# Performance work log

Measured on AMD Instinct MI355X. Metric: run time of the kernel, lower is better.

Reference implementation:

```python
import jax, jax.numpy as jnp
import numpy as np

B, S, HMODEL = 2, 4096, 2048
NH, HD, K = 16, 128, 4
RMS_EPS = 1e-5
L2_EPS = 1e-6


def setup_inputs() -> dict:
    key = jax.random.key(0)
    ks = jax.random.split(key, 10)
    def p(k, shape, std=0.02):
        return jax.random.normal(k, shape, jnp.float32) * std
    return {
        "x": jax.random.normal(ks[0], (B, S, HMODEL), jnp.float32),
        "Wq": p(ks[1], (NH * HD, HMODEL)),
        "Wk": p(ks[2], (NH * HD, HMODEL)),
        "Wv": p(ks[3], (NH * HD, HMODEL)),
        "Wb": p(ks[4], (NH, HMODEL)),
        "Wo": p(ks[5], (HMODEL, NH * HD)),
        "conv_q": p(ks[6], (NH * HD, K), 0.3),
        "conv_k": p(ks[7], (NH * HD, K), 0.3),
        "conv_v": p(ks[8], (NH * HD, K), 0.3),
        "rms_w": jnp.ones((HD,), jnp.float32),
    }


def causal_conv_silu(x, w):
    # depthwise causal conv1d: x [B,S,C], w [C,K]; out[t] = sum_i w[:,i]*x[t-K+1+i]
    Kw = w.shape[1]
    xp = jnp.pad(x, ((0, 0), (Kw - 1, 0), (0, 0)))
    out = sum(w[:, i] * xp[:, i:i + x.shape[1], :] for i in range(Kw))
    return jax.nn.silu(out)


def l2norm(x):
    return x * jax.lax.rsqrt(jnp.sum(x * x, axis=-1, keepdims=True) + L2_EPS)


def reference(x, Wq, Wk, Wv, Wb, Wo, conv_q, conv_k, conv_v, rms_w):
    b, s, _ = x.shape
    nh = Wb.shape[0]
    hd = Wq.shape[0] // nh

    q = causal_conv_silu(x @ Wq.T, conv_q)
    k = causal_conv_silu(x @ Wk.T, conv_k)
    v = causal_conv_silu(x @ Wv.T, conv_v)

    q = q.reshape(b, s, nh, hd)
    k = k.reshape(b, s, nh, hd)
    v = v.reshape(b, s, nh, hd)
    beta = jax.nn.sigmoid(x @ Wb.T)  # [B,S,NH]

    # qk l2 norm in kernel + default scale d_k^-0.5 on q
    q = l2norm(q) * (hd ** -0.5)
    k = l2norm(k)

    # delta rule recurrence: state [B,NH,HD,HD] (d_k x d_v)
    qT = jnp.moveaxis(q, 1, 0)  # [S,B,NH,HD]
    kT = jnp.moveaxis(k, 1, 0)
    vT = jnp.moveaxis(v, 1, 0)
    bT = jnp.moveaxis(beta, 1, 0)  # [S,B,NH]

    def step(state, inp):
        qt, kt, vt, bt = inp
        pred = jnp.einsum('bhd,bhdv->bhv', kt, state)
        delta = bt[..., None] * (vt - pred)
        state = state + jnp.einsum('bhd,bhv->bhdv', kt, delta)
        ot = jnp.einsum('bhd,bhdv->bhv', qt, state)
        return state, ot

    s0 = jnp.zeros((b, nh, hd, hd), x.dtype)
    _, o = jax.lax.scan(step, s0, (qT, kT, vT, bT))
    o = jnp.moveaxis(o, 0, 1)  # [B,S,NH,HD]

    # RMSNorm over head_dim
    o = o * jax.lax.rsqrt(jnp.mean(o * o, axis=-1, keepdims=True) + RMS_EPS) * rms_w

    o = o.reshape(b, s, nh * hd) @ Wo.T
    return o
```

## Files before the change

kernel.cpp:

```cpp
#include <hip/hip_runtime.h>

#define DI __device__ __forceinline__

constexpr int Bb = 2, Ss = 4096, Hm = 2048, NHh = 16, HDd = 128;
constexpr int ROWS = Bb * Ss;
constexpr int QKVN = 3 * Hm;
constexpr int CC = 64;
constexpr int NC = Ss / CC;

typedef __bf16 bf16x8 __attribute__((ext_vector_type(8)));
typedef float f32x4 __attribute__((ext_vector_type(4)));

DI unsigned short f2bf(float f) {
  unsigned int u = __float_as_uint(f);
  u = u + 0x7FFFu + ((u >> 16) & 1u);
  return (unsigned short)(u >> 16);
}
DI float bf2f(unsigned int u) { return __uint_as_float(u << 16); }
DI void ld_bf8(const unsigned short* p, float* f) {
  uint4 u = *(const uint4*)p;
  f[0] = bf2f(u.x & 0xffffu); f[1] = bf2f(u.x >> 16);
  f[2] = bf2f(u.y & 0xffffu); f[3] = bf2f(u.y >> 16);
  f[4] = bf2f(u.z & 0xffffu); f[5] = bf2f(u.z >> 16);
  f[6] = bf2f(u.w & 0xffffu); f[7] = bf2f(u.w >> 16);
}

DI void gld16(const unsigned short* g, unsigned short* l) {
  __builtin_amdgcn_global_load_lds(
      (const __attribute__((address_space(1))) unsigned int*)g,
      (__attribute__((address_space(3))) unsigned int*)l, 16, 0, 0);
}

DI void bar_lds() {
  asm volatile("s_waitcnt lgkmcnt(0)" ::: "memory");
  __builtin_amdgcn_s_barrier();
}

__global__ void cast_x_k(const float* __restrict__ x, unsigned short* __restrict__ xb) {
  int i = blockIdx.x * 256 + threadIdx.x;
  float4 f = ((const float4*)x)[i];
  ushort4 u;
  u.x = f2bf(f.x); u.y = f2bf(f.y); u.z = f2bf(f.z); u.w = f2bf(f.w);
  ((ushort4*)xb)[i] = u;
}

__global__ void cast_w_k(const float* __restrict__ Wq, const float* __restrict__ Wk,
                         const float* __restrict__ Wv, const float* __restrict__ Wo,
                         unsigned short* __restrict__ wqkv, unsigned short* __restrict__ wo) {
  const int W1 = Hm * Hm;
  int idx = blockIdx.x * 256 + threadIdx.x;
  for (int r = 0; r < 4; r++) {
    int i = idx + r * W1;
    if (i < W1)            wqkv[i] = f2bf(Wq[i]);
    else if (i < 2 * W1)   wqkv[i] = f2bf(Wk[i - W1]);
    else if (i < 3 * W1)   wqkv[i] = f2bf(Wv[i - 2 * W1]);
    else                   wo[i - 3 * W1] = f2bf(Wo[i - 3 * W1]);
  }
}

template <bool BF16_OUT>
__global__ __launch_bounds__(256) void gemm_bt(const unsigned short* __restrict__ A,
                                               const unsigned short* __restrict__ Bm,
                                               void* __restrict__ Cout,
                                               int M, int N, int Kd) {
  __shared__ __align__(16) unsigned short As[128 * 32];
  __shared__ __align__(16) unsigned short Bs[128 * 32];
  int tid = threadIdx.x;
  int bm = blockIdx.y * 128, bn = blockIdx.x * 128;
  int wave = tid >> 6, lane = tid & 63;
  int wm = (wave >> 1) * 64, wn = (wave & 1) * 64;
  int lm = lane & 15, lq = lane >> 4;
  f32x4 acc[4][4] = {};
  int sr = lane >> 2;
  int sc = (lane & 3) * 8;

  for (int k0 = 0; k0 < Kd; k0 += 32) {
    __syncthreads();
#pragma unroll
    for (int i = 0; i < 2; i++) {
      int inst = (wave << 1) + i;
      int r = inst * 16 + sr;
      gld16(&A[(size_t)(bm + r) * Kd + k0 + sc], &As[inst * 512]);
      gld16(&Bm[(size_t)(bn + r) * Kd + k0 + sc], &Bs[inst * 512]);
    }
    __syncthreads();
    bf16x8 af[4], bfr[4];
#pragma unroll
    for (int i = 0; i < 4; i++) af[i]  = *(const bf16x8*)&As[(wm + i * 16 + lm) * 32 + lq * 8];
#pragma unroll
    for (int j = 0; j < 4; j++) bfr[j] = *(const bf16x8*)&Bs[(wn + j * 16 + lm) * 32 + lq * 8];
#pragma unroll
    for (int i = 0; i < 4; i++)
#pragma unroll
      for (int j = 0; j < 4; j++)
        acc[i][j] = __builtin_amdgcn_mfma_f32_16x16x32_bf16(af[i], bfr[j], acc[i][j], 0, 0, 0);
  }
#pragma unroll
  for (int i = 0; i < 4; i++)
#pragma unroll
    for (int j = 0; j < 4; j++) {
      int row = bm + wm + i * 16 + lq * 4;
      int col = bn + wn + j * 16 + lm;
#pragma unroll
      for (int r = 0; r < 4; r++) {
        if (BF16_OUT)
          ((unsigned short*)Cout)[(size_t)(row + r) * N + col] = f2bf(acc[i][j][r]);
        else
          ((float*)Cout)[(size_t)(row + r) * N + col] = acc[i][j][r];
      }
    }
}

__global__ __launch_bounds__(256) void conv_k(const unsigned short* __restrict__ qkvh,
                                              const float* __restrict__ cwq,
                                              const float* __restrict__ cwk,
                                              const float* __restrict__ cwv,
                                              unsigned short* __restrict__ qb,
                                              unsigned short* __restrict__ kb,
                                              unsigned short* __restrict__ vb) {
  __shared__ __align__(16) float sm[32 * 260];
  __shared__ float fac[64];
  int tid = threadIdx.x;
  int cblk = blockIdx.x * 256;
  int s0 = blockIdx.y * 32;
  int z = blockIdx.z;
  int sel = z >> 1, b = z & 1;
  const float* cw = sel == 0 ? cwq : (sel == 1 ? cwk : cwv);
  int c = cblk + tid;
  float4 w = ((const float4*)cw)[c];
  const unsigned short* in = qkvh + (size_t)b * Ss * QKVN + sel * Hm + c;
  float x0 = (s0 >= 3) ? bf2f(in[(size_t)(s0 - 3) * QKVN]) : 0.f;
  float x1 = (s0 >= 2) ? bf2f(in[(size_t)(s0 - 2) * QKVN]) : 0.f;
  float x2 = (s0 >= 1) ? bf2f(in[(size_t)(s0 - 1) * QKVN]) : 0.f;
  for (int si = 0; si < 32; si++) {
    float x3 = bf2f(in[(size_t)(s0 + si) * QKVN]);
    float a = w.x * x0 + w.y * x1 + w.z * x2 + w.w * x3;
    sm[si * 260 + tid] = a / (1.f + __expf(-a));
    x0 = x1; x1 = x2; x2 = x3;
  }
  __syncthreads();
  if (sel < 2) {
    int si = tid >> 3, p = tid & 7;
    const float* row = &sm[si * 260 + p * 32];
    float ss = 0.f;
#pragma unroll
    for (int j = 0; j < 32; j += 4) {
      float4 v4 = *(const float4*)(row + j);
      ss += v4.x * v4.x + v4.y * v4.y + v4.z * v4.z + v4.w * v4.w;
    }
    ss += __shfl_xor(ss, 1);
    ss += __shfl_xor(ss, 2);
    float f = rsqrtf(ss + 1e-6f);
    if (sel == 0) f *= 0.08838834764831845f;
    if ((p & 3) == 0) fac[si * 2 + (p >> 2)] = f;
  }
  __syncthreads();
  unsigned short* outp = sel == 0 ? qb : (sel == 1 ? kb : vb);
  int hl = tid >> 7;
  for (int si = 0; si < 32; si++) {
    float val = sm[si * 260 + tid];
    if (sel < 2) val *= fac[si * 2 + hl];
    outp[(size_t)(b * Ss + s0 + si) * Hm + cblk + tid] = f2bf(val);
  }
}

__global__ __launch_bounds__(256) void beta_k(const float* __restrict__ x,
                                              const float* __restrict__ Wbm,
                                              float* __restrict__ beta) {
  int wid = threadIdx.x >> 6, lane = threadIdx.x & 63;
  int row = blockIdx.x * 4 + wid;
  int h = lane & 15, part = lane >> 4;
  const float* xr = x + (size_t)row * Hm + part * 512;
  const float* wr = Wbm + (size_t)h * Hm + part * 512;
  float acc = 0.f;
  for (int j = 0; j < 512; j += 4) {
    float4 xv = *(const float4*)(xr + j);
    float4 wv = *(const float4*)(wr + j);
    acc += xv.x * wv.x + xv.y * wv.y + xv.z * wv.z + xv.w * wv.w;
  }
  acc += __shfl_xor(acc, 16);
  acc += __shfl_xor(acc, 32);
  if (part == 0) beta[(size_t)row * NHh + h] = 1.f / (1.f + __expf(-acc));
}

__global__ __launch_bounds__(256) void recA_k(const unsigned short* __restrict__ qg,
                                              unsigned short* kg,
                                              const unsigned short* __restrict__ vg,
                                              const float* __restrict__ beta,
                                              unsigned short* __restrict__ Wo_,
                                              unsigned short* __restrict__ Uo,
                                              unsigned short* __restrict__ Kto) {
  __shared__ __align__(16) unsigned short Kc[64 * 136];
  __shared__ __align__(16) unsigned short Qc[64 * 136];
  __shared__ __align__(16) unsigned short Vt[128 * 72];
  __shared__ __align__(16) unsigned short Kt[128 * 72];
  __shared__ __align__(16) unsigned short Xa[64 * 72], Xat[64 * 72];
  __shared__ __align__(16) unsigned short Xb2[64 * 72], Xbt[64 * 72];
  __shared__ __align__(16) unsigned short Pa[64 * 72], Pb[64 * 72];
  __shared__ float bl[64];
  int tid = threadIdx.x;
  int c = blockIdx.x, bh = blockIdx.y;
  int b = bh >> 4, h = bh & 15;
  size_t cid = (size_t)bh * NC + c;
  size_t rowbase = (size_t)b * Ss + (size_t)c * CC;
  int wave = tid >> 6, lane = tid & 63, lm = lane & 15, lq = lane >> 4;

  for (int idx = tid; idx < 1024; idx += 256) {
    int r = idx >> 4, c8 = (idx & 15) * 8;
    *(uint4*)&Kc[r * 136 + c8] = *(const uint4*)&kg[(rowbase + r) * Hm + h * HDd + c8];
    *(uint4*)&Qc[r * 136 + c8] = *(const uint4*)&qg[(rowbase + r) * Hm + h * HDd + c8];
  }
  for (int idx = tid; idx < 8192; idx += 256) {
    int s = idx >> 7, vv = idx & 127;
    Vt[vv * 72 + s] = vg[(rowbase + s) * Hm + h * HDd + vv];
  }
  if (tid < 64) bl[tid] = beta[(rowbase + tid) * NHh + h];
  __syncthreads();

  for (int idx = tid; idx < 8192; idx += 256) {
    int s = idx >> 7, d = idx & 127;
    Kt[d * 72 + s] = Kc[s * 136 + d];
  }
  {
    f32x4 accA[4] = {};
#pragma unroll
    for (int kk = 0; kk < 4; kk++) {
      bf16x8 af = *(const bf16x8*)&Kc[(wave * 16 + lm) * 136 + kk * 32 + lq * 8];
#pragma unroll
      for (int st = 0; st < 4; st++) {
        bf16x8 bfr = *(const bf16x8*)&Kc[(st * 16 + lm) * 136 + kk * 32 + lq * 8];
        accA[st] = __builtin_amdgcn_mfma_f32_16x16x32_bf16(af, bfr, accA[st], 0, 0, 0);
      }
    }
#pragma unroll
    for (int st = 0; st < 4; st++)
#pragma unroll
      for (int r = 0; r < 4; r++) {
        int t = wave * 16 + lq * 4 + r, s = st * 16 + lm;
        float m = (t > s) ? -bl[t] * accA[st][r] : 0.f;
        unsigned short mb = f2bf(m);
        Xa[t * 72 + s] = mb;
        Xat[s * 72 + t] = mb;
        Pa[t * 72 + s] = (t == s) ? f2bf(1.f) : mb;
      }
  }
  {
    f32x4 accQ[4] = {};
#pragma unroll
    for (int kk = 0; kk < 4; kk++) {
      bf16x8 af = *(const bf16x8*)&Qc[(wave * 16 + lm) * 136 + kk * 32 + lq * 8];
#pragma unroll
      for (int st = 0; st < 4; st++) {
        bf16x8 bfr = *(const bf16x8*)&Kc[(st * 16 + lm) * 136 + kk * 32 + lq * 8];
        accQ[st] = __builtin_amdgcn_mfma_f32_16x16x32_bf16(af, bfr, accQ[st], 0, 0, 0);
      }
    }
#pragma unroll
    for (int st = 0; st < 4; st++)
#pragma unroll
      for (int r = 0; r < 4; r++) {
        int t = wave * 16 + lq * 4 + r, s = st * 16 + lm;
        kg[(rowbase + t) * Hm + h * HDd + s] = (s <= t) ? f2bf(accQ[st][r]) : (unsigned short)0;
      }
  }
  __syncthreads();

  unsigned short *X = Xa, *Xt = Xat, *Xn = Xb2, *Xnt = Xbt, *P = Pa, *Pn = Pb;
  for (int lvl = 1; lvl <= 5; lvl++) {
    f32x4 a1[4] = {}, a2[4] = {};
#pragma unroll
    for (int kk = 0; kk < 2; kk++) {
      bf16x8 afx  = *(const bf16x8*)&X[(wave * 16 + lm) * 72 + kk * 32 + lq * 8];
      bf16x8 afxt = *(const bf16x8*)&Xt[(wave * 16 + lm) * 72 + kk * 32 + lq * 8];
#pragma unroll
      for (int st = 0; st < 4; st++) {
        bf16x8 bx  = *(const bf16x8*)&X[(st * 16 + lm) * 72 + kk * 32 + lq * 8];
        bf16x8 bxt = *(const bf16x8*)&Xt[(st * 16 + lm) * 72 + kk * 32 + lq * 8];
        a1[st] = __builtin_amdgcn_mfma_f32_16x16x32_bf16(afx, bxt, a1[st], 0, 0, 0);
        a2[st] = __builtin_amdgcn_mfma_f32_16x16x32_bf16(afxt, bx, a2[st], 0, 0, 0);
      }
    }
#pragma unroll
    for (int st = 0; st < 4; st++)
#pragma unroll
      for (int r = 0; r < 4; r++) {
        int t = wave * 16 + lq * 4 + r, s = st * 16 + lm;
        Xn[t * 72 + s]  = f2bf(a1[st][r]);
        Xnt[t * 72 + s] = f2bf(a2[st][r]);
      }
    __syncthreads();
    f32x4 ap[4];
#pragma unroll
    for (int st = 0; st < 4; st++)
#pragma unroll
      for (int r = 0; r < 4; r++)
        ap[st][r] = bf2f(P[(wave * 16 + lq * 4 + r) * 72 + st * 16 + lm]);
#pragma unroll
    for (int kk = 0; kk < 2; kk++) {
      bf16x8 afp = *(const bf16x8*)&P[(wave * 16 + lm) * 72 + kk * 32 + lq * 8];
#pragma unroll
      for (int st = 0; st < 4; st++) {
        bf16x8 bxnt = *(const bf16x8*)&Xnt[(st * 16 + lm) * 72 + kk * 32 + lq * 8];
        ap[st] = __builtin_amdgcn_mfma_f32_16x16x32_bf16(afp, bxnt, ap[st], 0, 0, 0);
      }
    }
#pragma unroll
    for (int st = 0; st < 4; st++)
#pragma unroll
      for (int r = 0; r < 4; r++) {
        int t = wave * 16 + lq * 4 + r, s = st * 16 + lm;
        Pn[t * 72 + s] = f2bf((lvl == 5) ? ap[st][r] * bl[s] : ap[st][r]);
      }
    unsigned short* tmp;
    tmp = X; X = Xn; Xn = tmp;
    tmp = Xt; Xt = Xnt; Xnt = tmp;
    tmp = P; P = Pn; Pn = tmp;
    __syncthreads();
  }

  for (int idx = tid; idx < 1024; idx += 256) {
    int d = idx >> 3, s8 = (idx & 7) * 8;
    *(uint4*)&Kto[cid * 8192 + d * 64 + s8] = *(const uint4*)&Kt[d * 72 + s8];
  }
  {
    unsigned short* Up = Uo + cid * 8192;
    unsigned short* Wp = Wo_ + cid * 8192;
    f32x4 accU[8] = {}, accW[8] = {};
#pragma unroll
    for (int kk = 0; kk < 2; kk++) {
      bf16x8 af = *(const bf16x8*)&P[(wave * 16 + lm) * 72 + kk * 32 + lq * 8];
#pragma unroll
      for (int nt = 0; nt < 8; nt++) {
        bf16x8 bv = *(const bf16x8*)&Vt[(nt * 16 + lm) * 72 + kk * 32 + lq * 8];
        bf16x8 bk = *(const bf16x8*)&Kt[(nt * 16 + lm) * 72 + kk * 32 + lq * 8];
        accU[nt] = __builtin_amdgcn_mfma_f32_16x16x32_bf16(af, bv, accU[nt], 0, 0, 0);
        accW[nt] = __builtin_amdgcn_mfma_f32_16x16x32_bf16(af, bk, accW[nt], 0, 0, 0);
      }
    }
#pragma unroll
    for (int nt = 0; nt < 8; nt++)
#pragma unroll
      for (int r = 0; r < 4; r++) {
        int t = wave * 16 + lq * 4 + r, n = nt * 16 + lm;
        Up[t * 128 + n] = f2bf(accU[nt][r]);
        Wp[t * 128 + n] = f2bf(accW[nt][r]);
      }
  }
}

__global__ __launch_bounds__(256) void recB_k(const unsigned short* __restrict__ qg,
                                              const unsigned short* __restrict__ atg,
                                              const unsigned short* __restrict__ Wg,
                                              const unsigned short* __restrict__ Ug,
                                              const unsigned short* __restrict__ Ktg,
                                              unsigned short* __restrict__ og) {
  __shared__ __align__(16) unsigned short Wc[64 * 136];
  __shared__ __align__(16) unsigned short Qc[64 * 136];
  __shared__ __align__(16) unsigned short Ktc[128 * 72];
  __shared__ __align__(16) unsigned short Atc[64 * 72];
  __shared__ __align__(16) unsigned short Uc[64 * 24];
  __shared__ __align__(16) unsigned short Dt[16 * 72];
  __shared__ __align__(16) unsigned short Stb[16 * 136];
  __shared__ float St32[16 * 132];
  int tid = threadIdx.x;
  int lin = blockIdx.x + (blockIdx.y << 3);
  int xcd = lin & 7, slot = lin >> 3;
  int vs = slot & 7;
  int bh = xcd + ((slot >> 3) << 3);
  int b = bh >> 4, h = bh & 15, v0 = vs * 16;
  int wave = tid >> 6, lane = tid & 63, lm = lane & 15, lq = lane >> 4;

  for (int i = tid; i < 16 * 132; i += 256) St32[i] = 0.f;
  for (int i = tid; i < 16 * 136; i += 256) Stb[i] = 0;

  {
    size_t cid0 = (size_t)bh * NC;
    size_t rb0 = (size_t)b * Ss;
    const unsigned short* Wp = Wg + cid0 * 8192;
    const unsigned short* Ktp = Ktg + cid0 * 8192;
    const unsigned short* Up = Ug + cid0 * 8192 + v0;
#pragma unroll
    for (int j = 0; j < 4; j++) {
      int idx = tid + j * 256;
      int r = idx >> 4, c8 = (idx & 15) * 8;
      *(uint4*)&Wc[r * 136 + c8] = *(const uint4*)&Wp[r * 128 + c8];
      *(uint4*)&Qc[r * 136 + c8] = *(const uint4*)&qg[(rb0 + r) * Hm + h * HDd + c8];
      int r2 = idx >> 3, d8 = (idx & 7) * 8;
      *(uint4*)&Ktc[r2 * 72 + d8] = *(const uint4*)&Ktp[r2 * 64 + d8];
    }
#pragma unroll
    for (int j = 0; j < 2; j++) {
      int idx = tid + j * 256;
      int t = idx >> 3, s8 = (idx & 7) * 8;
      *(uint4*)&Atc[t * 72 + s8] = *(const uint4*)&atg[(rb0 + t) * Hm + h * HDd + s8];
    }
    if (tid < 128) {
      int t = tid >> 1, c8 = (tid & 1) * 8;
      *(uint4*)&Uc[t * 24 + c8] = *(const uint4*)&Up[t * 128 + c8];
    }
  }
  __syncthreads();

  for (int c = 0; c < NC; c++) {
    size_t rb = (size_t)b * Ss + (size_t)c * CC;
    int cn = (c + 1 < NC) ? c + 1 : c;
    size_t cidn = (size_t)bh * NC + cn;
    size_t rbn = (size_t)b * Ss + (size_t)cn * CC;
    const unsigned short* Wpn = Wg + cidn * 8192;
    const unsigned short* Ktpn = Ktg + cidn * 8192;
    const unsigned short* Upn = Ug + cidn * 8192 + v0;
    uint4 pw[4], pq[4], pk[4], pa[2], pu;
#pragma unroll
    for (int j = 0; j < 4; j++) {
      int idx = tid + j * 256;
      int r = idx >> 4, c8 = (idx & 15) * 8;
      pw[j] = *(const uint4*)&Wpn[r * 128 + c8];
      pq[j] = *(const uint4*)&qg[(rbn + r) * Hm + h * HDd + c8];
      int r2 = idx >> 3, d8 = (idx & 7) * 8;
      pk[j] = *(const uint4*)&Ktpn[r2 * 64 + d8];
    }
#pragma unroll
    for (int j = 0; j < 2; j++) {
      int idx = tid + j * 256;
      int t = idx >> 3, s8 = (idx & 7) * 8;
      pa[j] = *(const uint4*)&atg[(rbn + t) * Hm + h * HDd + s8];
    }
    if (tid < 128) {
      int t = tid >> 1, c8 = (tid & 1) * 8;
      pu = *(const uint4*)&Upn[t * 128 + c8];
    }

    {
      f32x4 accD = {};
#pragma unroll
      for (int kk = 0; kk < 4; kk++) {
        bf16x8 af = *(const bf16x8*)&Wc[(wave * 16 + lm) * 136 + kk * 32 + lq * 8];
        bf16x8 bfr = *(const bf16x8*)&Stb[lm * 136 + kk * 32 + lq * 8];
        accD = __builtin_amdgcn_mfma_f32_16x16x32_bf16(af, bfr, accD, 0, 0, 0);
      }
#pragma unroll
      for (int r = 0; r < 4; r++) {
        int t = wave * 16 + lq * 4 + r;
        float dv = bf2f(Uc[t * 24 + lm]) - accD[r];
        Dt[lm * 72 + t] = f2bf(dv);
      }
    }
    bar_lds();

    f32x4 accO = {};
    f32x4 accP[2] = {};
    {
#pragma unroll
      for (int kk = 0; kk < 4; kk++) {
        bf16x8 af = *(const bf16x8*)&Qc[(wave * 16 + lm) * 136 + kk * 32 + lq * 8];
        bf16x8 bfr = *(const bf16x8*)&Stb[lm * 136 + kk * 32 + lq * 8];
        accO = __builtin_amdgcn_mfma_f32_16x16x32_bf16(af, bfr, accO, 0, 0, 0);
      }
#pragma unroll
      for (int kk = 0; kk < 2; kk++) {
        bf16x8 af = *(const bf16x8*)&Atc[(wave * 16 + lm) * 72 + kk * 32 + lq * 8];
        bf16x8 bfr = *(const bf16x8*)&Dt[lm * 72 + kk * 32 + lq * 8];
        accO = __builtin_amdgcn_mfma_f32_16x16x32_bf16(af, bfr, accO, 0, 0, 0);
        bf16x8 afd = *(const bf16x8*)&Dt[lm * 72 + kk * 32 + lq * 8];
#pragma unroll
        for (int j = 0; j < 2; j++) {
          int dt = wave * 2 + j;
          bf16x8 bk = *(const bf16x8*)&Ktc[(dt * 16 + lm) * 72 + kk * 32 + lq * 8];
          accP[j] = __builtin_amdgcn_mfma_f32_16x16x32_bf16(afd, bk, accP[j], 0, 0, 0);
        }
      }
    }
    bar_lds();

#pragma unroll
    for (int r = 0; r < 4; r++) {
      int t = wave * 16 + lq * 4 + r;
      og[(rb + t) * Hm + h * HDd + v0 + lm] = f2bf(accO[r]);
    }
#pragma unroll
    for (int j = 0; j < 2; j++) {
      int dt = wave * 2 + j;
#pragma unroll
      for (int r = 0; r < 4; r++) {
        int vv = lq * 4 + r, d = dt * 16 + lm;
        float ns = St32[vv * 132 + d] + accP[j][r];
        St32[vv * 132 + d] = ns;
        Stb[vv * 136 + d] = f2bf(ns);
      }
    }
#pragma unroll
    for (int j = 0; j < 4; j++) {
      int idx = tid + j * 256;
      int r = idx >> 4, c8 = (idx & 15) * 8;
      *(uint4*)&Wc[r * 136 + c8] = pw[j];
      *(uint4*)&Qc[r * 136 + c8] = pq[j];
      int r2 = idx >> 3, d8 = (idx & 7) * 8;
      *(uint4*)&Ktc[r2 * 72 + d8] = pk[j];
    }
#pragma unroll
    for (int j = 0; j < 2; j++) {
      int idx = tid + j * 256;
      int t = idx >> 3, s8 = (idx & 7) * 8;
      *(uint4*)&Atc[t * 72 + s8] = pa[j];
    }
    if (tid < 128) {
      int t = tid >> 1, c8 = (tid & 1) * 8;
      *(uint4*)&Uc[t * 24 + c8] = pu;
    }
    bar_lds();
  }
}

__global__ __launch_bounds__(256) void rmsn_k(const unsigned short* __restrict__ o,
                                              const float* __restrict__ rw,
                                              unsigned short* __restrict__ ob) {
  int tid = threadIdx.x;
  size_t rowoff = (size_t)blockIdx.x * Hm + tid * 8;
  float f[8];
  ld_bf8(o + rowoff, f);
  float ss = f[0]*f[0] + f[1]*f[1] + f[2]*f[2] + f[3]*f[3] +
             f[4]*f[4] + f[5]*f[5] + f[6]*f[6] + f[7]*f[7];
  ss += __shfl_xor(ss, 1); ss += __shfl_xor(ss, 2); ss += __shfl_xor(ss, 4); ss += __shfl_xor(ss, 8);
  float sc = rsqrtf(ss * (1.f / 128.f) + 1e-5f);
  int d = (tid & 15) * 8;
  float4 wa = *(const float4*)(rw + d);
  float4 wb = *(const float4*)(rw + d + 4);
  ushort4 u0, u1;
  u0.x = f2bf(f[0] * sc * wa.x); u0.y = f2bf(f[1] * sc * wa.y);
  u0.z = f2bf(f[2] * sc * wa.z); u0.w = f2bf(f[3] * sc * wa.w);
  u1.x = f2bf(f[4] * sc * wb.x); u1.y = f2bf(f[5] * sc * wb.y);
  u1.z = f2bf(f[6] * sc * wb.z); u1.w = f2bf(f[7] * sc * wb.w);
  ((ushort4*)ob)[rowoff / 4] = u0;
  ((ushort4*)ob)[rowoff / 4 + 1] = u1;
}

extern "C" void kernel_launch(void* const* d_in, const int* in_sizes, int n_in,
                              void* d_out, int out_size, void* d_ws, size_t ws_size,
                              hipStream_t stream) {
  const float* x  = (const float*)d_in[0];
  const float* Wq = (const float*)d_in[1];
  const float* Wk = (const float*)d_in[2];
  const float* Wv = (const float*)d_in[3];
  const float* Wb = (const float*)d_in[4];
  const float* Wo = (const float*)d_in[5];
  const float* cq = (const float*)d_in[6];
  const float* ck = (const float*)d_in[7];
  const float* cv = (const float*)d_in[8];
  const float* rw = (const float*)d_in[9];

  unsigned short* xb  = (unsigned short*)d_out;
  unsigned short* vb  = (unsigned short*)d_out + (size_t)ROWS * Hm;
  unsigned short* o_b = (unsigned short*)d_out;
  float* out = (float*)d_out;

  char* ws = (char*)d_ws;
  size_t off = 0;
  auto alloc = [&](size_t bytes) {
    void* p = ws + off;
    off = (off + bytes + 255) & ~(size_t)255;
    return p;
  };
  unsigned short* wqkv = (unsigned short*)alloc((size_t)QKVN * Hm * 2);
  unsigned short* wob  = (unsigned short*)alloc((size_t)Hm * Hm * 2);
  unsigned short* qkvh = (unsigned short*)alloc((size_t)ROWS * QKVN * 2);
  unsigned short* qb   = (unsigned short*)alloc((size_t)ROWS * Hm * 2);
  unsigned short* kb   = (unsigned short*)alloc((size_t)ROWS * Hm * 2);
  float* beta          = (float*)alloc((size_t)ROWS * NHh * 4);
  unsigned short* Wch = qkvh;
  unsigned short* Uch = qkvh + (size_t)2048 * 8192;
  unsigned short* Kth = qkvh + (size_t)2 * 2048 * 8192;
  unsigned short* obb = qkvh;

  cast_x_k<<<ROWS * Hm / 1024, 256, 0, stream>>>(x, xb);
  cast_w_k<<<Hm * Hm / 256, 256, 0, stream>>>(Wq, Wk, Wv, Wo, wqkv, wob);
  gemm_bt<true><<<dim3(QKVN / 128, ROWS / 128), 256, 0, stream>>>(xb, wqkv, qkvh, ROWS, QKVN, Hm);
  beta_k<<<ROWS / 4, 256, 0, stream>>>(x, Wb, beta);
  conv_k<<<dim3(Hm / 256, Ss / 32, Bb * 3), 256, 0, stream>>>(qkvh, cq, ck, cv, qb, kb, vb);
  recA_k<<<dim3(NC, 32), 256, 0, stream>>>(qb, kb, vb, beta, Wch, Uch, Kth);
  recB_k<<<dim3(8, 32), 256, 0, stream>>>(qb, kb, Wch, Uch, Kth, o_b);
  rmsn_k<<<ROWS, 256, 0, stream>>>(o_b, rw, obb);
  gemm_bt<false><<<dim3(Hm / 128, ROWS / 128), 256, 0, stream>>>(obb, wob, out, ROWS, Hm, Hm);
}
```

Baseline: 1.020 ms.

## Replace GEMM with 256x256 tile, double-buffered, swizzled LDS pipelined kernel

Swaps the simple 128x128 single-buffer GEMM for a 512-thread 256x256-tile kernel with BK=64. It double-buffers LDS and interleaves global-to-LDS staging with four MFMA phases per K step, using explicit waitcnt, barriers and setprio. It also XOR-swizzles LDS rows to avoid bank conflicts and remaps workgroups for L2 locality. The aim is higher MFMA utilisation and less load latency in both projection GEMMs, at the cost of 128KB of LDS, heavy register use and fragile hand-written synchronisation.

```diff
diff --git a/kernel.cpp b/kernel.cpp
--- a/kernel.cpp
+++ b/kernel.cpp
@@ -58,55 +58,164 @@
   }
 }
 
+DI bf16x8 ldsw(const unsigned short* base, int r, int c16) {
+  return *(const bf16x8*)&base[r * 64 + ((c16 ^ (r & 7)) << 3)];
+}
+
 template <bool BF16_OUT>
-__global__ __launch_bounds__(256) void gemm_bt(const unsigned short* __restrict__ A,
+__global__ __launch_bounds__(512) void gemm256(const unsigned short* __restrict__ A,
                                                const unsigned short* __restrict__ Bm,
                                                void* __restrict__ Cout,
                                                int M, int N, int Kd) {
-  __shared__ __align__(16) unsigned short As[128 * 32];
-  __shared__ __align__(16) unsigned short Bs[128 * 32];
+  __shared__ __align__(16) unsigned short As[2][16384];
+  __shared__ __align__(16) unsigned short Bs[2][16384];
   int tid = threadIdx.x;
-  int bm = blockIdx.y * 128, bn = blockIdx.x * 128;
   int wave = tid >> 6, lane = tid & 63;
-  int wm = (wave >> 1) * 64, wn = (wave & 1) * 64;
   int lm = lane & 15, lq = lane >> 4;
-  f32x4 acc[4][4] = {};
-  int sr = lane >> 2;
-  int sc = (lane & 3) * 8;
-
-  for (int k0 = 0; k0 < Kd; k0 += 32) {
-    __syncthreads();
+  int wm = (wave >> 2) * 128, wn = (wave & 3) * 64;
+
+  int nx = N >> 8;
+  int nwg = gridDim.x * gridDim.y;
+  int lin = blockIdx.x + gridDim.x * blockIdx.y;
+  int cpx = nwg >> 3;
+  int swz = (lin & 7) * cpx + (lin >> 3);
+  int bn = (swz % nx) << 8, bm = (swz / nx) << 8;
+
+  int NT = Kd >> 6;
+  int rsub = lane >> 3;
+  int csw = ((lane & 7) ^ rsub) << 3;
+
+  auto stageA = [&](int buf, int half, int ts) {
+    int ksrc = (ts < NT ? ts : NT - 1) << 6;
 #pragma unroll
     for (int i = 0; i < 2; i++) {
-      int inst = (wave << 1) + i;
-      int r = inst * 16 + sr;
-      gld16(&A[(size_t)(bm + r) * Kd + k0 + sc], &As[inst * 512]);
-      gld16(&Bm[(size_t)(bn + r) * Kd + k0 + sc], &Bs[inst * 512]);
-    }
-    __syncthreads();
-    bf16x8 af[4], bfr[4];
-#pragma unroll
-    for (int i = 0; i < 4; i++) af[i]  = *(const bf16x8*)&As[(wm + i * 16 + lm) * 32 + lq * 8];
-#pragma unroll
-    for (int j = 0; j < 4; j++) bfr[j] = *(const bf16x8*)&Bs[(wn + j * 16 + lm) * 32 + lq * 8];
-#pragma unroll
-    for (int i = 0; i < 4; i++)
-#pragma unroll
-      for (int j = 0; j < 4; j++)
-        acc[i][j] = __builtin_amdgcn_mfma_f32_16x16x32_bf16(af[i], bfr[j], acc[i][j], 0, 0, 0);
-  }
-#pragma unroll
-  for (int i = 0; i < 4; i++)
-#pragma unroll
-    for (int j = 0; j < 4; j++) {
-      int row = bm + wm + i * 16 + lq * 4;
-      int col = bn + wn + j * 16 + lm;
+      int blk = wave * 2 + i;
+      int r = half * 128 + blk * 8 + rsub;
+      gld16(&A[(size_t)(bm + r) * Kd + ksrc + csw], &As[buf][half * 8192 + blk * 512]);
+    }
+  };
+  auto stageB = [&](int buf, int half, int ts) {
+    int ksrc = (ts < NT ? ts : NT - 1) << 6;
+#pragma unroll
+    for (int i = 0; i < 2; i++) {
+      int blk = wave * 2 + i;
+      int r = half * 128 + blk * 8 + rsub;
+      gld16(&Bm[(size_t)(bn + r) * Kd + ksrc + csw], &Bs[buf][half * 8192 + blk * 512]);
+    }
+  };
+
+  f32x4 acc[8][4] = {};
+  bf16x8 a[4][2], b[4][2];
+
+  stageA(0, 0, 0); stageA(0, 1, 0); stageB(0, 0, 0); stageB(0, 1, 0);
+  stageB(1, 0, 1); stageB(1, 1, 1);
+  asm volatile("s_waitcnt vmcnt(4)" ::: "memory");
+  __builtin_amdgcn_s_barrier();
+
+  for (int t = 0; t < NT; t++) {
+    int cur = t & 1, nxt = cur ^ 1;
+    const unsigned short* Ac = As[cur];
+    const unsigned short* Bc = Bs[cur];
+
+#pragma unroll
+    for (int fi = 0; fi < 4; fi++)
+#pragma unroll
+      for (int kk = 0; kk < 2; kk++)
+        a[fi][kk] = ldsw(Ac, wm + fi * 16 + lm, kk * 4 + lq);
+#pragma unroll
+    for (int fj = 0; fj < 2; fj++)
+#pragma unroll
+      for (int kk = 0; kk < 2; kk++)
+        b[fj][kk] = ldsw(Bc, wn + fj * 16 + lm, kk * 4 + lq);
+    stageA(nxt, 0, t + 1);
+    asm volatile("" ::: "memory");
+    __builtin_amdgcn_s_barrier();
+    asm volatile("s_waitcnt lgkmcnt(0)" ::: "memory");
+    __builtin_amdgcn_sched_barrier(0);
+    __builtin_amdgcn_s_setprio(1);
+#pragma unroll
+    for (int kk = 0; kk < 2; kk++)
+#pragma unroll
+      for (int fi = 0; fi < 4; fi++)
+#pragma unroll
+        for (int fj = 0; fj < 2; fj++)
+          acc[fi][fj] = __builtin_amdgcn_mfma_f32_16x16x32_bf16(a[fi][kk], b[fj][kk], acc[fi][fj], 0, 0, 0);
+    __builtin_amdgcn_s_setprio(0);
+    asm volatile("" ::: "memory");
+    __builtin_amdgcn_s_barrier();
+
+#pragma unroll
+    for (int fj = 0; fj < 2; fj++)
+#pragma unroll
+      for (int kk = 0; kk < 2; kk++)
+        b[2 + fj][kk] = ldsw(Bc, wn + (2 + fj) * 16 + lm, kk * 4 + lq);
+    stageA(nxt, 1, t + 1);
+    asm volatile("" ::: "memory");
+    __builtin_amdgcn_s_barrier();
+    asm volatile("s_waitcnt lgkmcnt(0)" ::: "memory");
+    __builtin_amdgcn_sched_barrier(0);
+    __builtin_amdgcn_s_setprio(1);
+#pragma unroll
+    for (int kk = 0; kk < 2; kk++)
+#pragma unroll
+      for (int fi = 0; fi < 4; fi++)
+#pragma unroll
+        for (int fj = 0; fj < 2; fj++)
+          acc[fi][2 + fj] = __builtin_amdgcn_mfma_f32_16x16x32_bf16(a[fi][kk], b[2 + fj][kk], acc[fi][2 + fj], 0, 0, 0);
+    __builtin_amdgcn_s_setprio(0);
+    asm volatile("" ::: "memory");
+    __builtin_amdgcn_s_barrier();
+
+#pragma unroll
+    for (int fi = 0; fi < 4; fi++)
+#pragma unroll
+      for (int kk = 0; kk < 2; kk++)
+        a[fi][kk] = ldsw(Ac, wm + 64 + fi * 16 + lm, kk * 4 + lq);
+    stageB(cur, 0, t + 2);
+    asm volatile("" ::: "memory");
+    __builtin_amdgcn_s_barrier();
+    asm volatile("s_waitcnt lgkmcnt(0)" ::: "memory");
+    __builtin_amdgcn_sched_barrier(0);
+    __builtin_amdgcn_s_setprio(1);
+#pragma unroll
+    for (int kk = 0; kk < 2; kk++)
+#pragma unroll
+      for (int fi = 0; fi < 4; fi++)
+#pragma unroll
+        for (int fj = 0; fj < 2; fj++)
+          acc[4 + fi][2 + fj] = __builtin_amdgcn_mfma_f32_16x16x32_bf16(a[fi][kk], b[2 + fj][kk], acc[4 + fi][2 + fj], 0, 0, 0);
+    __builtin_amdgcn_s_setprio(0);
+    asm volatile("" ::: "memory");
+    __builtin_amdgcn_s_barrier();
+
+    stageB(cur, 1, t + 2);
+    asm volatile("" ::: "memory");
+    __builtin_amdgcn_s_barrier();
+    __builtin_amdgcn_s_setprio(1);
+#pragma unroll
+    for (int kk = 0; kk < 2; kk++)
+#pragma unroll
+      for (int fi = 0; fi < 4; fi++)
+#pragma unroll
+        for (int fj = 0; fj < 2; fj++)
+          acc[4 + fi][fj] = __builtin_amdgcn_mfma_f32_16x16x32_bf16(a[fi][kk], b[fj][kk], acc[4 + fi][fj], 0, 0, 0);
+    __builtin_amdgcn_s_setprio(0);
+    asm volatile("s_waitcnt vmcnt(4)" ::: "memory");
+    __builtin_amdgcn_s_barrier();
+  }
+
+#pragma unroll
+  for (int fi = 0; fi < 8; fi++)
+#pragma unroll
+    for (int fj = 0; fj < 4; fj++) {
+      int row = bm + wm + fi * 16 + lq * 4;
+      int col = bn + wn + fj * 16 + lm;
 #pragma unroll
       for (int r = 0; r < 4; r++) {
         if (BF16_OUT)
-          ((unsigned short*)Cout)[(size_t)(row + r) * N + col] = f2bf(acc[i][j][r]);
+          ((unsigned short*)Cout)[(size_t)(row + r) * N + col] = f2bf(acc[fi][fj][r]);
         else
-          ((float*)Cout)[(size_t)(row + r) * N + col] = acc[i][j][r];
+          ((float*)Cout)[(size_t)(row + r) * N + col] = acc[fi][fj][r];
       }
     }
 }
@@ -573,11 +682,11 @@
 
   cast_x_k<<<ROWS * Hm / 1024, 256, 0, stream>>>(x, xb);
   cast_w_k<<<Hm * Hm / 256, 256, 0, stream>>>(Wq, Wk, Wv, Wo, wqkv, wob);
-  gemm_bt<true><<<dim3(QKVN / 128, ROWS / 128), 256, 0, stream>>>(xb, wqkv, qkvh, ROWS, QKVN, Hm);
+  gemm256<true><<<dim3(QKVN / 256, ROWS / 256), 512, 0, stream>>>(xb, wqkv, qkvh, ROWS, QKVN, Hm);
   beta_k<<<ROWS / 4, 256, 0, stream>>>(x, Wb, beta);
   conv_k<<<dim3(Hm / 256, Ss / 32, Bb * 3), 256, 0, stream>>>(qkvh, cq, ck, cv, qb, kb, vb);
   recA_k<<<dim3(NC, 32), 256, 0, stream>>>(qb, kb, vb, beta, Wch, Uch, Kth);
   recB_k<<<dim3(8, 32), 256, 0, stream>>>(qb, kb, Wch, Uch, Kth, o_b);
   rmsn_k<<<ROWS, 256, 0, stream>>>(o_b, rw, obb);
-  gemm_bt<false><<<dim3(Hm / 128, ROWS / 128), 256, 0, stream>>>(obb, wob, out, ROWS, Hm, Hm);
-}
+  gemm256<false><<<dim3(Hm / 256, ROWS / 256), 512, 0, stream>>>(obb, wob, out, ROWS, Hm, Hm);
+}
```

Measured after the change: 964.0 us. -5.5%, faster.
